# Kernel optimization log

Hardware: AMD Instinct MI355X
Metric: run time of the kernel (lower is better)

Reference implementation:

```python
import jax, jax.numpy as jnp
import numpy as np

B, D, H, W = 16, 512, 32, 32
M = 2000
TEMP_UPDATE = 0.1
TEMP_GATHER = 0.1


def l2norm(x, axis, eps=1e-12):
    # matches F.normalize: x / max(||x||_2, eps)
    n = jnp.linalg.norm(x, axis=axis, keepdims=True)
    return x / jnp.maximum(n, eps)


def setup_inputs() -> dict:
    key = jax.random.key(0)
    k1, k2 = jax.random.split(key)
    query = jax.random.normal(k1, (B, D, H, W), dtype=jnp.float32)
    # memory bank initialized as F.normalize(randn) * 0.1, as in __init__
    keys = l2norm(jax.random.normal(k2, (M, D), dtype=jnp.float32), axis=1) * 0.1
    return {"query": query, "keys": keys}


def reference(query, keys):
    b, d, h, w = query.shape
    m = keys.shape[0]
    # normalize along channels, move to [B,H,W,D], flatten to [N,D]
    q = jnp.transpose(l2norm(query, axis=1), (0, 2, 3, 1))
    qf = q.reshape(b * h * w, d)  # [N, D]

    # --- get_score (same score reused by gather_loss / read / update) ---
    score = l2norm(qf, axis=1) @ l2norm(keys, axis=1).T  # [N, M] cosine sims
    tg = min(max(TEMP_GATHER, 1e-8), 1.0)
    tu = min(max(TEMP_UPDATE, 1e-8), 1.0)
    score_query = jax.nn.softmax(score / tg, axis=0)   # softmax over queries
    score_memory = jax.nn.softmax(score / tu, axis=1)  # softmax over memory slots

    # --- gather_loss (train) ---
    _, top2 = jax.lax.top_k(score_memory, 2)  # [N, 2]
    pos = jax.lax.stop_gradient(keys[top2[:, 0]])
    neg = jax.lax.stop_gradient(keys[top2[:, 1]])
    compactness_loss = jnp.mean((qf - pos) ** 2)
    # TripletMarginLoss(margin=1.0), torch pairwise_distance eps=1e-6
    dp = jnp.sqrt(jnp.sum((qf - pos + 1e-6) ** 2, axis=-1))
    dn = jnp.sqrt(jnp.sum((qf - neg + 1e-6) ** 2, axis=-1))
    separateness_loss = jnp.mean(jnp.maximum(dp - dn + 1.0, 0.0))

    # --- read ---
    concat_memory = jax.lax.stop_gradient(score_memory) @ keys  # [N, D]
    updated_query = jnp.concatenate([qf, concat_memory], axis=1)
    updated_query = jnp.transpose(updated_query.reshape(b, h, w, 2 * d), (0, 3, 1, 2))

    # --- update (vectorized get_update_query: per-slot gather + weighted sum) ---
    g = top2[:, 0]  # top-1 gathering index per query, [N]
    col_max = jnp.max(score_query, axis=0)  # [M]
    w_raw = jnp.take_along_axis(score_query, g[:, None], axis=1)[:, 0] / (col_max[g] + 1e-8)
    denom = jax.ops.segment_sum(w_raw, g, num_segments=m) + 1e-8  # [M]
    weights = w_raw / denom[g]
    query_update = jax.ops.segment_sum(weights[:, None] * qf, g, num_segments=m)  # [M, D]
    updated_memory = jax.lax.stop_gradient(l2norm(query_update + keys, axis=1))

    return (updated_query, updated_memory, score_query, score_memory,
            separateness_loss, compactness_loss)
```

## Files before the change

### kernel.cpp

```cpp
#include <hip/hip_runtime.h>
#include <math.h>

#define NQ 16384
#define DD 512
#define MM 2000
#define MPAD 2048
#define KPAD 2048

#define UQ_OFF   0
#define UM_OFF   16777216
#define SQ_OFF   17801216
#define SM_OFF   50569216
#define SEP_OFF  83337216
#define COMP_OFF 83337217

typedef unsigned short u16;
typedef __attribute__((ext_vector_type(8))) short bhalf8;
typedef __attribute__((ext_vector_type(4))) float f32x4;

__device__ float    g_qf[NQ * DD];
__device__ float    g_keyshat[MM * DD];
__device__ float    g_invn[NQ];
__device__ int      g_top1[NQ];
__device__ int      g_top2[NQ];
__device__ unsigned g_colmax[MM];
__device__ float    g_colsum[MM];
__device__ float    g_wraw[NQ];
__device__ float    g_denom[MM];
__device__ float    g_bins[128];
__device__ int      g_cnt[MM];
__device__ int      g_cursor[MM];
__device__ int      g_base[MM];
__device__ int      g_rows[NQ];
__device__ float    g_wvals[NQ];

__device__ __attribute__((aligned(16))) u16 g_qh[NQ * DD];
__device__ __attribute__((aligned(16))) u16 g_ql[NQ * DD];
__device__ __attribute__((aligned(16))) u16 g_kh[MPAD * DD];
__device__ __attribute__((aligned(16))) u16 g_kl[MPAD * DD];
__device__ __attribute__((aligned(16))) u16 g_kth[DD * KPAD];
__device__ __attribute__((aligned(16))) u16 g_ktl[DD * KPAD];
__device__ __attribute__((aligned(16))) u16 g_smh[(size_t)NQ * KPAD];
__device__ __attribute__((aligned(16))) u16 g_sml[(size_t)NQ * KPAD];

__device__ inline u16 f32_to_bf16(float x) {
    unsigned u = __float_as_uint(x);
    return (u16)((u + 0x7fffu + ((u >> 16) & 1u)) >> 16);
}
__device__ inline float bf16f(u16 h) { return __uint_as_float((unsigned)h << 16); }

__global__ __launch_bounds__(256) void init_kernel() {
    int i = blockIdx.x * 256 + threadIdx.x;
    if (i < MM) { g_colsum[i] = 0.f; g_denom[i] = 0.f; g_colmax[i] = 0u;
                  g_cnt[i] = 0; g_cursor[i] = 0; }
    if (i < 128) g_bins[i] = 0.f;
}

__global__ __launch_bounds__(256) void keys_norm_kernel(const float* __restrict__ keys) {
    int m = blockIdx.x, t = threadIdx.x;
    float v0 = keys[m * DD + t], v1 = keys[m * DD + t + 256];
    __shared__ float red[256];
    red[t] = v0 * v0 + v1 * v1;
    __syncthreads();
    for (int s = 128; s > 0; s >>= 1) { if (t < s) red[t] += red[t + s]; __syncthreads(); }
    float inv = 1.f / fmaxf(sqrtf(red[0]), 1e-12f);
    float n0 = v0 * inv, n1 = v1 * inv;
    g_keyshat[m * DD + t]       = n0;
    g_keyshat[m * DD + t + 256] = n1;
    u16 h0 = f32_to_bf16(n0), h1 = f32_to_bf16(n1);
    g_kh[(size_t)m * DD + t]       = h0;
    g_kl[(size_t)m * DD + t]       = f32_to_bf16(n0 - bf16f(h0));
    g_kh[(size_t)m * DD + t + 256] = h1;
    g_kl[(size_t)m * DD + t + 256] = f32_to_bf16(n1 - bf16f(h1));
}

__global__ __launch_bounds__(256) void ktrans_kernel(const float* __restrict__ keys) {
    __shared__ float tile[32][33];
    int tx = threadIdx.x & 31, ty = threadIdx.x >> 5;
    int c0 = blockIdx.x * 32;
    int m0 = blockIdx.y * 32;
    for (int i = ty; i < 32; i += 8) {
        int m = m0 + i;
        tile[i][tx] = (m < MM) ? keys[(size_t)m * DD + c0 + tx] : 0.f;
    }
    __syncthreads();
    for (int i = ty; i < 32; i += 8) {
        int c = c0 + i;
        float v = tile[tx][i];
        u16 h = f32_to_bf16(v);
        g_kth[(size_t)c * KPAD + m0 + tx] = h;
        g_ktl[(size_t)c * KPAD + m0 + tx] = f32_to_bf16(v - bf16f(h));
    }
}

__global__ __launch_bounds__(256) void qnorm_kernel(const float* __restrict__ q) {
    int bh = blockIdx.x; int b = bh >> 5, h = bh & 31;
    int t = threadIdx.x; int w = t & 31, dl = t >> 5;
    const float* qb = q + (size_t)b * DD * 1024 + h * 32;

    float ss = 0.f;
    for (int d = dl; d < DD; d += 8) { float v = qb[d * 1024 + w]; ss = fmaf(v, v, ss); }
    __shared__ float red[8][32];
    __shared__ float sinv[32];
    red[dl][w] = ss;
    __syncthreads();
    if (dl == 0) {
        float tot = 0.f;
        #pragma unroll
        for (int j = 0; j < 8; ++j) tot += red[j][w];
        float inv = 1.f / fmaxf(sqrtf(tot), 1e-12f);
        sinv[w] = inv;
        g_invn[b * 1024 + h * 32 + w] = inv;
    }
    __syncthreads();

    __shared__ float tile[32][33];
    int dcol = t & 31, wl = t >> 5;
    for (int d0 = 0; d0 < DD; d0 += 32) {
        for (int dd = dl; dd < 32; dd += 8)
            tile[dd][w] = qb[(d0 + dd) * 1024 + w] * sinv[w];
        __syncthreads();
        for (int wr = wl; wr < 32; wr += 8) {
            float v = tile[dcol][wr];
            size_t idx = ((size_t)b * 1024 + h * 32 + wr) * DD + d0 + dcol;
            g_qf[idx] = v;
            u16 hh = f32_to_bf16(v);
            g_qh[idx] = hh;
            g_ql[idx] = f32_to_bf16(v - bf16f(hh));
        }
        __syncthreads();
    }
}

__global__ __launch_bounds__(256) void qf_out_kernel(const float* __restrict__ q, float* __restrict__ out) {
    int e0 = blockIdx.x * 1024 + threadIdx.x;
    #pragma unroll
    for (int i = 0; i < 4; ++i) {
        int e = e0 + i * 256;
        int b = e >> 19;
        int rem = e & ((1 << 19) - 1);
        int c = rem >> 10, r = rem & 1023;
        out[UQ_OFF + (size_t)(b * 1024 + c) * 1024 + r] = q[e] * g_invn[b * 1024 + r];
    }
}

__device__ inline void mfma_block(const u16 (*Ah)[64], const u16 (*Al)[64],
                                  const u16 (*Bh)[64], const u16 (*Bl)[64],
                                  int wr, int wc, int l15, int hi, f32x4 acc[4][4]) {
    for (int sub = 0; sub < 2; ++sub) {
        bhalf8 a_h[4], a_l[4], b_h[4], b_l[4];
        #pragma unroll
        for (int i = 0; i < 4; ++i) {
            int r = wr + i * 16 + l15;
            int ps = (((sub << 2) | hi) ^ (r & 7)) << 3;
            a_h[i] = *(const bhalf8*)&Ah[r][ps];
            a_l[i] = *(const bhalf8*)&Al[r][ps];
        }
        #pragma unroll
        for (int j = 0; j < 4; ++j) {
            int c = wc + j * 16 + l15;
            int ps = (((sub << 2) | hi) ^ (c & 7)) << 3;
            b_h[j] = *(const bhalf8*)&Bh[c][ps];
            b_l[j] = *(const bhalf8*)&Bl[c][ps];
        }
        #pragma unroll
        for (int i = 0; i < 4; ++i)
            #pragma unroll
            for (int j = 0; j < 4; ++j) {
                acc[i][j] = __builtin_amdgcn_mfma_f32_16x16x32_bf16(a_h[i], b_h[j], acc[i][j], 0, 0, 0);
                acc[i][j] = __builtin_amdgcn_mfma_f32_16x16x32_bf16(a_h[i], b_l[j], acc[i][j], 0, 0, 0);
                acc[i][j] = __builtin_amdgcn_mfma_f32_16x16x32_bf16(a_l[i], b_h[j], acc[i][j], 0, 0, 0);
            }
    }
}

__global__ __launch_bounds__(256, 2) void gemm1_mfma(float* __restrict__ out) {
    __shared__ __attribute__((aligned(16))) u16 Ah[128][64];
    __shared__ __attribute__((aligned(16))) u16 Al[128][64];
    __shared__ __attribute__((aligned(16))) u16 Bh[128][64];
    __shared__ __attribute__((aligned(16))) u16 Bl[128][64];
    int t = threadIdx.x;
    int lane = t & 63, wid = t >> 6;
    int wr = (wid >> 1) << 6, wc = (wid & 1) << 6;
    int l15 = lane & 15, hi = lane >> 4;
    int row0 = blockIdx.x * 128;
    int col0 = blockIdx.y * 128;

    f32x4 acc[4][4] = {};
    int sr = t >> 3, sslot = t & 7;

    for (int k0 = 0; k0 < DD; k0 += 64) {
        #pragma unroll
        for (int pass = 0; pass < 4; ++pass) {
            int r = sr + pass * 32;
            int ps = (sslot ^ (r & 7)) << 3;
            size_t ga = (size_t)(row0 + r) * DD + k0 + sslot * 8;
            size_t gb = (size_t)(col0 + r) * DD + k0 + sslot * 8;
            *(uint4*)&Ah[r][ps] = *(const uint4*)&g_qh[ga];
            *(uint4*)&Al[r][ps] = *(const uint4*)&g_ql[ga];
            *(uint4*)&Bh[r][ps] = *(const uint4*)&g_kh[gb];
            *(uint4*)&Bl[r][ps] = *(const uint4*)&g_kl[gb];
        }
        __syncthreads();
        mfma_block(Ah, Al, Bh, Bl, wr, wc, l15, hi, acc);
        __syncthreads();
    }
    #pragma unroll
    for (int i = 0; i < 4; ++i) {
        int rbase = row0 + wr + i * 16 + hi * 4;
        #pragma unroll
        for (int j = 0; j < 4; ++j) {
            int c = col0 + wc + j * 16 + l15;
            if (c < MM) {
                #pragma unroll
                for (int q = 0; q < 4; ++q)
                    out[SQ_OFF + (size_t)(rbase + q) * MM + c] = acc[i][j][q];
            }
        }
    }
}

__global__ __launch_bounds__(256) void row_softmax_kernel(float* __restrict__ out) {
    int n = blockIdx.x, t = threadIdx.x;
    __shared__ float buf[MM];
    __shared__ float rv[256], rv2[256];
    __shared__ int   ri[256], ri2[256];

    const float* raw = out + SQ_OFF + (size_t)n * MM;
    float v1 = -3.0e38f, v2 = -3.0e38f; int i1 = 0x7fffffff, i2 = 0x7fffffff;
    #pragma unroll
    for (int i = 0; i < 8; ++i) {
        int idx = i * 256 + t;
        if (idx < MM) {
            float v = raw[idx];
            buf[idx] = v;
            if (v > v1)      { v2 = v1; i2 = i1; v1 = v; i1 = idx; }
            else if (v > v2) { v2 = v; i2 = idx; }
        }
    }
    rv[t] = v1; ri[t] = i1; rv2[t] = v2; ri2[t] = i2;
    __syncthreads();
    for (int s = 128; s > 0; s >>= 1) {
        if (t < s) {
            float av1 = rv[t],  bv1 = rv[t + s];
            float av2 = rv2[t], bv2 = rv2[t + s];
            int   ai1 = ri[t],  bi1 = ri[t + s];
            int   ai2 = ri2[t], bi2 = ri2[t + s];
            bool afirst = (av1 > bv1) || (av1 == bv1 && ai1 < bi1);
            float nv1, nv2; int ni1, ni2;
            if (afirst) {
                nv1 = av1; ni1 = ai1;
                if ((av2 > bv1) || (av2 == bv1 && ai2 < bi1)) { nv2 = av2; ni2 = ai2; }
                else                                          { nv2 = bv1; ni2 = bi1; }
            } else {
                nv1 = bv1; ni1 = bi1;
                if ((bv2 > av1) || (bv2 == av1 && bi2 < ai1)) { nv2 = bv2; ni2 = bi2; }
                else                                          { nv2 = av1; ni2 = ai1; }
            }
            rv[t] = nv1; ri[t] = ni1; rv2[t] = nv2; ri2[t] = ni2;
        }
        __syncthreads();
    }
    float rowmax = rv[0];
    if (t == 0) { g_top1[n] = ri[0]; g_top2[n] = ri2[0]; }
    __syncthreads();

    float lsum = 0.f;
    #pragma unroll
    for (int i = 0; i < 8; ++i) {
        int idx = i * 256 + t;
        if (idx < MM) {
            float e = expf((buf[idx] - rowmax) * 10.0f);
            buf[idx] = e;
            lsum += e;
        }
    }
    rv[t] = lsum;
    __syncthreads();
    for (int s = 128; s > 0; s >>= 1) { if (t < s) rv[t] += rv[t + s]; __syncthreads(); }
    float inv = 1.f / rv[0];
    float* sm = out + SM_OFF + (size_t)n * MM;
    #pragma unroll
    for (int i = 0; i < 8; ++i) {
        int idx = i * 256 + t;
        if (idx < MM) {
            float smv = buf[idx] * inv;
            sm[idx] = smv;
            u16 hh = f32_to_bf16(smv);
            g_smh[(size_t)n * KPAD + idx] = hh;
            g_sml[(size_t)n * KPAD + idx] = f32_to_bf16(smv - bf16f(hh));
        }
    }
}

__global__ __launch_bounds__(256) void rerank_kernel() {
    int n = blockIdx.x * 4 + (threadIdx.x >> 6);
    int lane = threadIdx.x & 63;
    int i1 = g_top1[n], i2 = g_top2[n];
    const float* q  = g_qf      + (size_t)n  * DD;
    const float* k1 = g_keyshat + (size_t)i1 * DD;
    const float* k2 = g_keyshat + (size_t)i2 * DD;
    float s1 = 0.f, s2 = 0.f;
    for (int k = lane; k < DD; k += 64) {
        float qv = q[k];
        s1 = fmaf(qv, k1[k], s1);
        s2 = fmaf(qv, k2[k], s2);
    }
    #pragma unroll
    for (int off = 32; off > 0; off >>= 1) {
        s1 += __shfl_down(s1, off);
        s2 += __shfl_down(s2, off);
    }
    if (lane == 0) {
        if (s2 > s1 || (s2 == s1 && i2 < i1)) { g_top1[n] = i2; g_top2[n] = i1; }
    }
}

__global__ __launch_bounds__(256) void col_stats_kernel(const float* __restrict__ out) {
    int m = blockIdx.x * 256 + threadIdx.x;
    if (m >= MM) return;
    int n0 = blockIdx.y * 256;
    const float* raw = out + SQ_OFF;
    float lmax = 0.f, lsum = 0.f;
    for (int i = 0; i < 256; ++i) {
        float v = raw[(size_t)(n0 + i) * MM + m];
        float e = expf((v - 1.0f) * 10.0f);
        lmax = fmaxf(lmax, e);
        lsum += e;
    }
    atomicMax(&g_colmax[m], __float_as_uint(lmax));
    atomicAdd(&g_colsum[m], lsum);
}

__global__ __launch_bounds__(256) void score_query_kernel(float* __restrict__ out) {
    int m = blockIdx.x * 256 + threadIdx.x;
    if (m >= MM) return;
    int n0 = blockIdx.y * 8;
    float inv = 1.f / g_colsum[m];
    float* raw = out + SQ_OFF;
    #pragma unroll
    for (int i = 0; i < 8; ++i) {
        size_t idx = (size_t)(n0 + i) * MM + m;
        raw[idx] = expf((raw[idx] - 1.0f) * 10.0f) * inv;
    }
}

__global__ __launch_bounds__(256) void wraw_kernel(const float* __restrict__ out) {
    int n = blockIdx.x * 256 + threadIdx.x;
    int gi = g_top1[n];
    float sqv = out[SQ_OFF + (size_t)n * MM + gi];
    float cm = __uint_as_float(g_colmax[gi]) / g_colsum[gi];
    float w = sqv / (cm + 1e-8f);
    g_wraw[n] = w;
    atomicAdd(&g_denom[gi], w);
    atomicAdd(&g_cnt[gi], 1);
}

__global__ __launch_bounds__(256) void scan_kernel() {
    int t = threadIdx.x;
    __shared__ int chunk[256];
    __shared__ int off[256];
    int loc[8];
    int s = 0;
    #pragma unroll
    for (int i = 0; i < 8; ++i) {
        int idx = t * 8 + i;
        int c = (idx < MM) ? g_cnt[idx] : 0;
        loc[i] = s; s += c;
    }
    chunk[t] = s;
    __syncthreads();
    if (t == 0) {
        int acc = 0;
        for (int i = 0; i < 256; ++i) { off[i] = acc; acc += chunk[i]; }
    }
    __syncthreads();
    #pragma unroll
    for (int i = 0; i < 8; ++i) {
        int idx = t * 8 + i;
        if (idx < MM) g_base[idx] = off[t] + loc[i];
    }
}

__global__ __launch_bounds__(256) void scatter_kernel() {
    int n = blockIdx.x * 256 + threadIdx.x;
    int gi = g_top1[n];
    int pos = atomicAdd(&g_cursor[gi], 1);
    int dst = g_base[gi] + pos;
    g_rows[dst]  = n;
    g_wvals[dst] = g_wraw[n];
}

__global__ __launch_bounds__(256) void seg_update_kernel(const float* __restrict__ keys, float* __restrict__ out) {
    int m = blockIdx.x, t = threadIdx.x;
    int start = g_base[m], cnt = g_cnt[m];
    float invd = 1.f / (g_denom[m] + 1e-8f);
    float acc0 = 0.f, acc1 = 0.f;
    for (int i = 0; i < cnt; ++i) {
        int   row = g_rows[start + i];
        float wgt = g_wvals[start + i] * invd;
        acc0 = fmaf(wgt, g_qf[(size_t)row * DD + t],       acc0);
        acc1 = fmaf(wgt, g_qf[(size_t)row * DD + t + 256], acc1);
    }
    float v0 = acc0 + keys[m * DD + t];
    float v1 = acc1 + keys[m * DD + t + 256];
    __shared__ float red[256];
    red[t] = v0 * v0 + v1 * v1;
    __syncthreads();
    for (int s = 128; s > 0; s >>= 1) { if (t < s) red[t] += red[t + s]; __syncthreads(); }
    float inv = 1.f / fmaxf(sqrtf(red[0]), 1e-12f);
    out[UM_OFF + (size_t)m * DD + t]       = v0 * inv;
    out[UM_OFF + (size_t)m * DD + t + 256] = v1 * inv;
}

__global__ __launch_bounds__(256, 2) void gemm2_mfma(float* __restrict__ out) {
    __shared__ __attribute__((aligned(16))) u16 Ah[128][64];
    __shared__ __attribute__((aligned(16))) u16 Al[128][64];
    __shared__ __attribute__((aligned(16))) u16 Bh[128][64];
    __shared__ __attribute__((aligned(16))) u16 Bl[128][64];
    int t = threadIdx.x;
    int lane = t & 63, wid = t >> 6;
    int wr = (wid >> 1) << 6, wc = (wid & 1) << 6;
    int l15 = lane & 15, hi = lane >> 4;
    int row0 = blockIdx.x * 128;
    int col0 = blockIdx.y * 128;

    f32x4 acc[4][4] = {};
    int sr = t >> 3, sslot = t & 7;

    for (int k0 = 0; k0 < KPAD; k0 += 64) {
        #pragma unroll
        for (int pass = 0; pass < 4; ++pass) {
            int r = sr + pass * 32;
            int ps = (sslot ^ (r & 7)) << 3;
            size_t ga = (size_t)(row0 + r) * KPAD + k0 + sslot * 8;
            size_t gb = (size_t)(col0 + r) * KPAD + k0 + sslot * 8;
            *(uint4*)&Ah[r][ps] = *(const uint4*)&g_kth[ga];
            *(uint4*)&Al[r][ps] = *(const uint4*)&g_ktl[ga];
            *(uint4*)&Bh[r][ps] = *(const uint4*)&g_smh[gb];
            *(uint4*)&Bl[r][ps] = *(const uint4*)&g_sml[gb];
        }
        __syncthreads();
        mfma_block(Ah, Al, Bh, Bl, wr, wc, l15, hi, acc);
        __syncthreads();
    }
    int bq = col0 >> 10;
    #pragma unroll
    for (int i = 0; i < 4; ++i) {
        int chb = row0 + wr + i * 16 + hi * 4;
        #pragma unroll
        for (int j = 0; j < 4; ++j) {
            int n = col0 + wc + j * 16 + l15;
            size_t base = UQ_OFF + ((size_t)(bq * 1024 + 512 + chb)) * 1024 + (n & 1023);
            #pragma unroll
            for (int q = 0; q < 4; ++q)
                out[base + (size_t)q * 1024] = acc[i][j][q];
        }
    }
}

__global__ __launch_bounds__(256) void loss_kernel(const float* __restrict__ keys) {
    int n = blockIdx.x, t = threadIdx.x;
    int gi = g_top1[n], ni = g_top2[n];
    float q0 = g_qf[(size_t)n * DD + t],      q1 = g_qf[(size_t)n * DD + t + 256];
    float p0 = keys[gi * DD + t],             p1 = keys[gi * DD + t + 256];
    float e0 = keys[ni * DD + t],             e1 = keys[ni * DD + t + 256];
    float dq0 = q0 - p0, dq1 = q1 - p1;
    float comp = dq0 * dq0 + dq1 * dq1;
    float a0 = dq0 + 1e-6f, a1 = dq1 + 1e-6f;
    float dpp = a0 * a0 + a1 * a1;
    float b0 = q0 - e0 + 1e-6f, b1 = q1 - e1 + 1e-6f;
    float dnn = b0 * b0 + b1 * b1;
    __shared__ float r1[256], r2[256], r3[256];
    r1[t] = comp; r2[t] = dpp; r3[t] = dnn;
    __syncthreads();
    for (int s = 128; s > 0; s >>= 1) {
        if (t < s) { r1[t] += r1[t + s]; r2[t] += r2[t + s]; r3[t] += r3[t + s]; }
        __syncthreads();
    }
    if (t == 0) {
        float dp = sqrtf(r2[0]), dn = sqrtf(r3[0]);
        float sep = fmaxf(dp - dn + 1.0f, 0.0f);
        atomicAdd(&g_bins[n & 63], sep);
        atomicAdd(&g_bins[64 + (n & 63)], r1[0]);
    }
}

__global__ __launch_bounds__(64) void finalize_kernel(float* __restrict__ out) {
    if (threadIdx.x == 0) {
        float s = 0.f, c = 0.f;
        for (int i = 0; i < 64; ++i) { s += g_bins[i]; c += g_bins[64 + i]; }
        out[SEP_OFF]  = s / (float)NQ;
        out[COMP_OFF] = c / ((float)NQ * (float)DD);
    }
}

extern "C" void kernel_launch(void* const* d_in, const int* in_sizes, int n_in,
                              void* d_out, int out_size, void* d_ws, size_t ws_size,
                              hipStream_t stream) {
    const float* query = (const float*)d_in[0];
    const float* keys  = (const float*)d_in[1];
    float* out = (float*)d_out;

    init_kernel<<<dim3(8), dim3(256), 0, stream>>>();
    keys_norm_kernel<<<dim3(MM), dim3(256), 0, stream>>>(keys);
    ktrans_kernel<<<dim3(16, 63), dim3(256), 0, stream>>>(keys);
    qnorm_kernel<<<dim3(512), dim3(256), 0, stream>>>(query);
    qf_out_kernel<<<dim3(8192), dim3(256), 0, stream>>>(query, out);
    gemm1_mfma<<<dim3(128, 16), dim3(256), 0, stream>>>(out);
    row_softmax_kernel<<<dim3(NQ), dim3(256), 0, stream>>>(out);
    rerank_kernel<<<dim3(NQ / 4), dim3(256), 0, stream>>>();
    col_stats_kernel<<<dim3(8, 64), dim3(256), 0, stream>>>(out);
    score_query_kernel<<<dim3(8, 2048), dim3(256), 0, stream>>>(out);
    wraw_kernel<<<dim3(64), dim3(256), 0, stream>>>(out);
    scan_kernel<<<dim3(1), dim3(256), 0, stream>>>();
    scatter_kernel<<<dim3(64), dim3(256), 0, stream>>>();
    seg_update_kernel<<<dim3(MM), dim3(256), 0, stream>>>(keys, out);
    gemm2_mfma<<<dim3(4, 128), dim3(256), 0, stream>>>(out);
    loss_kernel<<<dim3(NQ), dim3(256), 0, stream>>>(keys);
    finalize_kernel<<<dim3(1), dim3(64), 0, stream>>>(out);
}
```

Measured before the change: 1.026 ms.

## Fuse exp and row/column stats into GEMM epilogue and merge passes

The score GEMM epilogue now computes exp((s-1)*10) directly, using the fact that cosine scores are at most 1, and accumulates row sums and column sums/maxes through atomics. This lets the separate column-stats and score-query passes be folded into one row pass, and removes several full reads and writes of the large score matrix. The normalized-query output is written inside qnorm, the loss is merged into rerank, and GEMM tile loads switch to direct global-to-LDS loads. The cost is many more atomics and a fixed max shift that relies on scores never exceeding 1.

```diff
diff --git a/kernel.cpp b/kernel.cpp
--- a/kernel.cpp
+++ b/kernel.cpp
@@ -20,11 +20,11 @@
 
 __device__ float    g_qf[NQ * DD];
 __device__ float    g_keyshat[MM * DD];
-__device__ float    g_invn[NQ];
 __device__ int      g_top1[NQ];
 __device__ int      g_top2[NQ];
 __device__ unsigned g_colmax[MM];
 __device__ float    g_colsum[MM];
+__device__ float    g_rowsum[NQ];
 __device__ float    g_wraw[NQ];
 __device__ float    g_denom[MM];
 __device__ float    g_bins[128];
@@ -49,11 +49,18 @@
 }
 __device__ inline float bf16f(u16 h) { return __uint_as_float((unsigned)h << 16); }
 
+__device__ __forceinline__ void gl_lds16(const void* g, void* l) {
+    __builtin_amdgcn_global_load_lds(
+        (const __attribute__((address_space(1))) void*)g,
+        (__attribute__((address_space(3))) void*)l, 16, 0, 0);
+}
+
 __global__ __launch_bounds__(256) void init_kernel() {
     int i = blockIdx.x * 256 + threadIdx.x;
     if (i < MM) { g_colsum[i] = 0.f; g_denom[i] = 0.f; g_colmax[i] = 0u;
                   g_cnt[i] = 0; g_cursor[i] = 0; }
     if (i < 128) g_bins[i] = 0.f;
+    if (i < NQ) g_rowsum[i] = 0.f;
 }
 
 __global__ __launch_bounds__(256) void keys_norm_kernel(const float* __restrict__ keys) {
@@ -93,7 +100,7 @@
     }
 }
 
-__global__ __launch_bounds__(256) void qnorm_kernel(const float* __restrict__ q) {
+__global__ __launch_bounds__(256) void qnorm_kernel(const float* __restrict__ q, float* __restrict__ out) {
     int bh = blockIdx.x; int b = bh >> 5, h = bh & 31;
     int t = threadIdx.x; int w = t & 31, dl = t >> 5;
     const float* qb = q + (size_t)b * DD * 1024 + h * 32;
@@ -108,17 +115,18 @@
         float tot = 0.f;
         #pragma unroll
         for (int j = 0; j < 8; ++j) tot += red[j][w];
-        float inv = 1.f / fmaxf(sqrtf(tot), 1e-12f);
-        sinv[w] = inv;
-        g_invn[b * 1024 + h * 32 + w] = inv;
+        sinv[w] = 1.f / fmaxf(sqrtf(tot), 1e-12f);
     }
     __syncthreads();
 
     __shared__ float tile[32][33];
     int dcol = t & 31, wl = t >> 5;
     for (int d0 = 0; d0 < DD; d0 += 32) {
-        for (int dd = dl; dd < 32; dd += 8)
-            tile[dd][w] = qb[(d0 + dd) * 1024 + w] * sinv[w];
+        for (int dd = dl; dd < 32; dd += 8) {
+            float v = qb[(d0 + dd) * 1024 + w] * sinv[w];
+            tile[dd][w] = v;
+            out[UQ_OFF + (size_t)((b << 10) + d0 + dd) * 1024 + (h << 5) + w] = v;
+        }
         __syncthreads();
         for (int wr = wl; wr < 32; wr += 8) {
             float v = tile[dcol][wr];
@@ -132,18 +140,6 @@
     }
 }
 
-__global__ __launch_bounds__(256) void qf_out_kernel(const float* __restrict__ q, float* __restrict__ out) {
-    int e0 = blockIdx.x * 1024 + threadIdx.x;
-    #pragma unroll
-    for (int i = 0; i < 4; ++i) {
-        int e = e0 + i * 256;
-        int b = e >> 19;
-        int rem = e & ((1 << 19) - 1);
-        int c = rem >> 10, r = rem & 1023;
-        out[UQ_OFF + (size_t)(b * 1024 + c) * 1024 + r] = q[e] * g_invn[b * 1024 + r];
-    }
-}
-
 __device__ inline void mfma_block(const u16 (*Ah)[64], const u16 (*Al)[64],
                                   const u16 (*Bh)[64], const u16 (*Bl)[64],
                                   int wr, int wc, int l15, int hi, f32x4 acc[4][4]) {
@@ -180,62 +176,95 @@
     __shared__ __attribute__((aligned(16))) u16 Bh[128][64];
     __shared__ __attribute__((aligned(16))) u16 Bl[128][64];
     int t = threadIdx.x;
-    int lane = t & 63, wid = t >> 6;
-    int wr = (wid >> 1) << 6, wc = (wid & 1) << 6;
+    int lane = t & 63, wv = t >> 6;
+    int wr = (wv >> 1) << 6, wc = (wv & 1) << 6;
     int l15 = lane & 15, hi = lane >> 4;
     int row0 = blockIdx.x * 128;
     int col0 = blockIdx.y * 128;
 
     f32x4 acc[4][4] = {};
-    int sr = t >> 3, sslot = t & 7;
+    int lr = lane >> 3, sslot = lane & 7;
+    int xs = sslot ^ lr;
 
     for (int k0 = 0; k0 < DD; k0 += 64) {
         #pragma unroll
-        for (int pass = 0; pass < 4; ++pass) {
-            int r = sr + pass * 32;
-            int ps = (sslot ^ (r & 7)) << 3;
-            size_t ga = (size_t)(row0 + r) * DD + k0 + sslot * 8;
-            size_t gb = (size_t)(col0 + r) * DD + k0 + sslot * 8;
-            *(uint4*)&Ah[r][ps] = *(const uint4*)&g_qh[ga];
-            *(uint4*)&Al[r][ps] = *(const uint4*)&g_ql[ga];
-            *(uint4*)&Bh[r][ps] = *(const uint4*)&g_kh[gb];
-            *(uint4*)&Bl[r][ps] = *(const uint4*)&g_kl[gb];
+        for (int p = 0; p < 4; ++p) {
+            int r = wv * 8 + lr + p * 32;
+            size_t ga = (size_t)(row0 + r) * DD + k0 + xs * 8;
+            size_t gb = (size_t)(col0 + r) * DD + k0 + xs * 8;
+            gl_lds16(g_qh + ga, &Ah[p * 32 + wv * 8][0]);
+            gl_lds16(g_ql + ga, &Al[p * 32 + wv * 8][0]);
+            gl_lds16(g_kh + gb, &Bh[p * 32 + wv * 8][0]);
+            gl_lds16(g_kl + gb, &Bl[p * 32 + wv * 8][0]);
         }
         __syncthreads();
         mfma_block(Ah, Al, Bh, Bl, wr, wc, l15, hi, acc);
         __syncthreads();
     }
-    #pragma unroll
-    for (int i = 0; i < 4; ++i) {
-        int rbase = row0 + wr + i * 16 + hi * 4;
-        #pragma unroll
-        for (int j = 0; j < 4; ++j) {
-            int c = col0 + wc + j * 16 + l15;
-            if (c < MM) {
-                #pragma unroll
-                for (int q = 0; q < 4; ++q)
-                    out[SQ_OFF + (size_t)(rbase + q) * MM + c] = acc[i][j][q];
+
+    float rowp[4][4];
+    #pragma unroll
+    for (int i = 0; i < 4; ++i)
+        #pragma unroll
+        for (int q = 0; q < 4; ++q) rowp[i][q] = 0.f;
+
+    #pragma unroll
+    for (int j = 0; j < 4; ++j) {
+        int c = col0 + wc + j * 16 + l15;
+        bool valid = (c < MM);
+        float cs = 0.f, cm = 0.f;
+        #pragma unroll
+        for (int i = 0; i < 4; ++i) {
+            int rbase = row0 + wr + i * 16 + hi * 4;
+            #pragma unroll
+            for (int q = 0; q < 4; ++q) {
+                float e = __expf((acc[i][j][q] - 1.0f) * 10.0f);
+                if (valid) out[SQ_OFF + (size_t)(rbase + q) * MM + c] = e;
+                float ev = valid ? e : 0.f;
+                rowp[i][q] += ev;
+                cs += ev;
+                cm = fmaxf(cm, ev);
             }
         }
-    }
-}
-
-__global__ __launch_bounds__(256) void row_softmax_kernel(float* __restrict__ out) {
+        cs += __shfl_xor(cs, 16); cs += __shfl_xor(cs, 32);
+        cm = fmaxf(cm, __shfl_xor(cm, 16)); cm = fmaxf(cm, __shfl_xor(cm, 32));
+        if (hi == 0 && valid) {
+            atomicAdd(&g_colsum[c], cs);
+            atomicMax(&g_colmax[c], __float_as_uint(cm));
+        }
+    }
+    #pragma unroll
+    for (int i = 0; i < 4; ++i)
+        #pragma unroll
+        for (int q = 0; q < 4; ++q) {
+            float v = rowp[i][q];
+            v += __shfl_xor(v, 1); v += __shfl_xor(v, 2);
+            v += __shfl_xor(v, 4); v += __shfl_xor(v, 8);
+            if (l15 == 0) atomicAdd(&g_rowsum[row0 + wr + i * 16 + hi * 4 + q], v);
+        }
+}
+
+__global__ __launch_bounds__(256) void rowpass_kernel(float* __restrict__ out) {
     int n = blockIdx.x, t = threadIdx.x;
-    __shared__ float buf[MM];
     __shared__ float rv[256], rv2[256];
     __shared__ int   ri[256], ri2[256];
-
-    const float* raw = out + SQ_OFF + (size_t)n * MM;
-    float v1 = -3.0e38f, v2 = -3.0e38f; int i1 = 0x7fffffff, i2 = 0x7fffffff;
+    float inv_rs = 1.f / g_rowsum[n];
+    float* raw = out + SQ_OFF + (size_t)n * MM;
+    float* sm  = out + SM_OFF + (size_t)n * MM;
+    float v1 = -1.f, v2 = -1.f; int i1 = 0x7fffffff, i2 = 0x7fffffff;
     #pragma unroll
     for (int i = 0; i < 8; ++i) {
         int idx = i * 256 + t;
         if (idx < MM) {
-            float v = raw[idx];
-            buf[idx] = v;
-            if (v > v1)      { v2 = v1; i2 = i1; v1 = v; i1 = idx; }
-            else if (v > v2) { v2 = v; i2 = idx; }
+            float e = raw[idx];
+            if (e > v1)      { v2 = v1; i2 = i1; v1 = e; i1 = idx; }
+            else if (e > v2) { v2 = e; i2 = idx; }
+            float smv = e * inv_rs;
+            sm[idx] = smv;
+            u16 hh = f32_to_bf16(smv);
+            g_smh[(size_t)n * KPAD + idx] = hh;
+            g_sml[(size_t)n * KPAD + idx] = f32_to_bf16(smv - bf16f(hh));
+            raw[idx] = e / g_colsum[idx];
         }
     }
     rv[t] = v1; ri[t] = i1; rv2[t] = v2; ri2[t] = i2;
@@ -261,39 +290,10 @@
         }
         __syncthreads();
     }
-    float rowmax = rv[0];
     if (t == 0) { g_top1[n] = ri[0]; g_top2[n] = ri2[0]; }
-    __syncthreads();
-
-    float lsum = 0.f;
-    #pragma unroll
-    for (int i = 0; i < 8; ++i) {
-        int idx = i * 256 + t;
-        if (idx < MM) {
-            float e = expf((buf[idx] - rowmax) * 10.0f);
-            buf[idx] = e;
-            lsum += e;
-        }
-    }
-    rv[t] = lsum;
-    __syncthreads();
-    for (int s = 128; s > 0; s >>= 1) { if (t < s) rv[t] += rv[t + s]; __syncthreads(); }
-    float inv = 1.f / rv[0];
-    float* sm = out + SM_OFF + (size_t)n * MM;
-    #pragma unroll
-    for (int i = 0; i < 8; ++i) {
-        int idx = i * 256 + t;
-        if (idx < MM) {
-            float smv = buf[idx] * inv;
-            sm[idx] = smv;
-            u16 hh = f32_to_bf16(smv);
-            g_smh[(size_t)n * KPAD + idx] = hh;
-            g_sml[(size_t)n * KPAD + idx] = f32_to_bf16(smv - bf16f(hh));
-        }
-    }
-}
-
-__global__ __launch_bounds__(256) void rerank_kernel() {
+}
+
+__global__ __launch_bounds__(256) void rerank_loss_kernel(const float* __restrict__ keys) {
     int n = blockIdx.x * 4 + (threadIdx.x >> 6);
     int lane = threadIdx.x & 63;
     int i1 = g_top1[n], i2 = g_top2[n];
@@ -301,47 +301,45 @@
     const float* k1 = g_keyshat + (size_t)i1 * DD;
     const float* k2 = g_keyshat + (size_t)i2 * DD;
     float s1 = 0.f, s2 = 0.f;
-    for (int k = lane; k < DD; k += 64) {
+    #pragma unroll
+    for (int kk = 0; kk < 8; ++kk) {
+        int k = lane + kk * 64;
         float qv = q[k];
         s1 = fmaf(qv, k1[k], s1);
         s2 = fmaf(qv, k2[k], s2);
     }
     #pragma unroll
-    for (int off = 32; off > 0; off >>= 1) {
-        s1 += __shfl_down(s1, off);
-        s2 += __shfl_down(s2, off);
+    for (int off = 1; off < 64; off <<= 1) {
+        s1 += __shfl_xor(s1, off);
+        s2 += __shfl_xor(s2, off);
+    }
+    bool sw = (s2 > s1) || (s2 == s1 && i2 < i1);
+    int gi = sw ? i2 : i1, ni = sw ? i1 : i2;
+    if (lane == 0 && sw) { g_top1[n] = i2; g_top2[n] = i1; }
+    const float* kp = keys + (size_t)gi * DD;
+    const float* kn = keys + (size_t)ni * DD;
+    float comp = 0.f, dpp = 0.f, dnn = 0.f;
+    #pragma unroll
+    for (int kk = 0; kk < 8; ++kk) {
+        int k = lane + kk * 64;
+        float qv = q[k];
+        float dq = qv - kp[k];
+        comp = fmaf(dq, dq, comp);
+        float a = dq + 1e-6f;
+        dpp = fmaf(a, a, dpp);
+        float b2 = qv - kn[k] + 1e-6f;
+        dnn = fmaf(b2, b2, dnn);
+    }
+    #pragma unroll
+    for (int off = 1; off < 64; off <<= 1) {
+        comp += __shfl_xor(comp, off);
+        dpp  += __shfl_xor(dpp,  off);
+        dnn  += __shfl_xor(dnn,  off);
     }
     if (lane == 0) {
-        if (s2 > s1 || (s2 == s1 && i2 < i1)) { g_top1[n] = i2; g_top2[n] = i1; }
-    }
-}
-
-__global__ __launch_bounds__(256) void col_stats_kernel(const float* __restrict__ out) {
-    int m = blockIdx.x * 256 + threadIdx.x;
-    if (m >= MM) return;
-    int n0 = blockIdx.y * 256;
-    const float* raw = out + SQ_OFF;
-    float lmax = 0.f, lsum = 0.f;
-    for (int i = 0; i < 256; ++i) {
-        float v = raw[(size_t)(n0 + i) * MM + m];
-        float e = expf((v - 1.0f) * 10.0f);
-        lmax = fmaxf(lmax, e);
-        lsum += e;
-    }
-    atomicMax(&g_colmax[m], __float_as_uint(lmax));
-    atomicAdd(&g_colsum[m], lsum);
-}
-
-__global__ __launch_bounds__(256) void score_query_kernel(float* __restrict__ out) {
-    int m = blockIdx.x * 256 + threadIdx.x;
-    if (m >= MM) return;
-    int n0 = blockIdx.y * 8;
-    float inv = 1.f / g_colsum[m];
-    float* raw = out + SQ_OFF;
-    #pragma unroll
-    for (int i = 0; i < 8; ++i) {
-        size_t idx = (size_t)(n0 + i) * MM + m;
-        raw[idx] = expf((raw[idx] - 1.0f) * 10.0f) * inv;
+        float dp = sqrtf(dpp), dn = sqrtf(dnn);
+        atomicAdd(&g_bins[n & 63], fmaxf(dp - dn + 1.0f, 0.0f));
+        atomicAdd(&g_bins[64 + (n & 63)], comp);
     }
 }
 
@@ -419,26 +417,26 @@
     __shared__ __attribute__((aligned(16))) u16 Bh[128][64];
     __shared__ __attribute__((aligned(16))) u16 Bl[128][64];
     int t = threadIdx.x;
-    int lane = t & 63, wid = t >> 6;
-    int wr = (wid >> 1) << 6, wc = (wid & 1) << 6;
+    int lane = t & 63, wv = t >> 6;
+    int wr = (wv >> 1) << 6, wc = (wv & 1) << 6;
     int l15 = lane & 15, hi = lane >> 4;
     int row0 = blockIdx.x * 128;
     int col0 = blockIdx.y * 128;
 
     f32x4 acc[4][4] = {};
-    int sr = t >> 3, sslot = t & 7;
+    int lr = lane >> 3, sslot = lane & 7;
+    int xs = sslot ^ lr;
 
     for (int k0 = 0; k0 < KPAD; k0 += 64) {
         #pragma unroll
-        for (int pass = 0; pass < 4; ++pass) {
-            int r = sr + pass * 32;
-            int ps = (sslot ^ (r & 7)) << 3;
-            size_t ga = (size_t)(row0 + r) * KPAD + k0 + sslot * 8;
-            size_t gb = (size_t)(col0 + r) * KPAD + k0 + sslot * 8;
-            *(uint4*)&Ah[r][ps] = *(const uint4*)&g_kth[ga];
-            *(uint4*)&Al[r][ps] = *(const uint4*)&g_ktl[ga];
-            *(uint4*)&Bh[r][ps] = *(const uint4*)&g_smh[gb];
-            *(uint4*)&Bl[r][ps] = *(const uint4*)&g_sml[gb];
+        for (int p = 0; p < 4; ++p) {
+            int r = wv * 8 + lr + p * 32;
+            size_t ga = (size_t)(row0 + r) * KPAD + k0 + xs * 8;
+            size_t gb = (size_t)(col0 + r) * KPAD + k0 + xs * 8;
+            gl_lds16(g_kth + ga, &Ah[p * 32 + wv * 8][0]);
+            gl_lds16(g_ktl + ga, &Al[p * 32 + wv * 8][0]);
+            gl_lds16(g_smh + gb, &Bh[p * 32 + wv * 8][0]);
+            gl_lds16(g_sml + gb, &Bl[p * 32 + wv * 8][0]);
         }
         __syncthreads();
         mfma_block(Ah, Al, Bh, Bl, wr, wc, l15, hi, acc);
@@ -459,33 +457,6 @@
     }
 }
 
-__global__ __launch_bounds__(256) void loss_kernel(const float* __restrict__ keys) {
-    int n = blockIdx.x, t = threadIdx.x;
-    int gi = g_top1[n], ni = g_top2[n];
-    float q0 = g_qf[(size_t)n * DD + t],      q1 = g_qf[(size_t)n * DD + t + 256];
-    float p0 = keys[gi * DD + t],             p1 = keys[gi * DD + t + 256];
-    float e0 = keys[ni * DD + t],             e1 = keys[ni * DD + t + 256];
-    float dq0 = q0 - p0, dq1 = q1 - p1;
-    float comp = dq0 * dq0 + dq1 * dq1;
-    float a0 = dq0 + 1e-6f, a1 = dq1 + 1e-6f;
-    float dpp = a0 * a0 + a1 * a1;
-    float b0 = q0 - e0 + 1e-6f, b1 = q1 - e1 + 1e-6f;
-    float dnn = b0 * b0 + b1 * b1;
-    __shared__ float r1[256], r2[256], r3[256];
-    r1[t] = comp; r2[t] = dpp; r3[t] = dnn;
-    __syncthreads();
-    for (int s = 128; s > 0; s >>= 1) {
-        if (t < s) { r1[t] += r1[t + s]; r2[t] += r2[t + s]; r3[t] += r3[t + s]; }
-        __syncthreads();
-    }
-    if (t == 0) {
-        float dp = sqrtf(r2[0]), dn = sqrtf(r3[0]);
-        float sep = fmaxf(dp - dn + 1.0f, 0.0f);
-        atomicAdd(&g_bins[n & 63], sep);
-        atomicAdd(&g_bins[64 + (n & 63)], r1[0]);
-    }
-}
-
 __global__ __launch_bounds__(64) void finalize_kernel(float* __restrict__ out) {
     if (threadIdx.x == 0) {
         float s = 0.f, c = 0.f;
@@ -502,21 +473,17 @@
     const float* keys  = (const float*)d_in[1];
     float* out = (float*)d_out;
 
-    init_kernel<<<dim3(8), dim3(256), 0, stream>>>();
+    init_kernel<<<dim3(64), dim3(256), 0, stream>>>();
     keys_norm_kernel<<<dim3(MM), dim3(256), 0, stream>>>(keys);
     ktrans_kernel<<<dim3(16, 63), dim3(256), 0, stream>>>(keys);
-    qnorm_kernel<<<dim3(512), dim3(256), 0, stream>>>(query);
-    qf_out_kernel<<<dim3(8192), dim3(256), 0, stream>>>(query, out);
+    qnorm_kernel<<<dim3(512), dim3(256), 0, stream>>>(query, out);
     gemm1_mfma<<<dim3(128, 16), dim3(256), 0, stream>>>(out);
-    row_softmax_kernel<<<dim3(NQ), dim3(256), 0, stream>>>(out);
-    rerank_kernel<<<dim3(NQ / 4), dim3(256), 0, stream>>>();
-    col_stats_kernel<<<dim3(8, 64), dim3(256), 0, stream>>>(out);
-    score_query_kernel<<<dim3(8, 2048), dim3(256), 0, stream>>>(out);
+    rowpass_kernel<<<dim3(NQ), dim3(256), 0, stream>>>(out);
+    rerank_loss_kernel<<<dim3(NQ / 4), dim3(256), 0, stream>>>(keys);
     wraw_kernel<<<dim3(64), dim3(256), 0, stream>>>(out);
     scan_kernel<<<dim3(1), dim3(256), 0, stream>>>();
     scatter_kernel<<<dim3(64), dim3(256), 0, stream>>>();
     seg_update_kernel<<<dim3(MM), dim3(256), 0, stream>>>(keys, out);
     gemm2_mfma<<<dim3(4, 128), dim3(256), 0, stream>>>(out);
-    loss_kernel<<<dim3(NQ), dim3(256), 0, stream>>>(keys);
     finalize_kernel<<<dim3(1), dim3(64), 0, stream>>>(out);
 }
```

Result: faster. 971.9 us (-5.3%).
